# Kernel optimization log

Hardware: AMD Instinct MI355X
Metric: run time of the kernel (lower is better)

The kernel has to match this reference:

```python
import jax, jax.numpy as jnp
import numpy as np

B, N, C = 4, 2048, 768
H = 12
HD = C // H

def setup_inputs() -> dict:
    key = jax.random.key(0)
    k1, k2, k3, k4, k5 = jax.random.split(key, 5)
    x = jax.random.normal(k1, (B, N, C), dtype=jnp.float32)
    qkv_w = jax.random.normal(k2, (3 * C, C), dtype=jnp.float32) * (1.0 / np.sqrt(C))
    qkv_b = jax.random.normal(k3, (3 * C,), dtype=jnp.float32) * 0.02
    proj_w = jax.random.normal(k4, (C, C), dtype=jnp.float32) * (1.0 / np.sqrt(C))
    proj_b = jax.random.normal(k5, (C,), dtype=jnp.float32) * 0.02
    return {"x": x, "qkv_w": qkv_w, "qkv_b": qkv_b, "proj_w": proj_w, "proj_b": proj_b}

def reference(x, qkv_w, qkv_b, proj_w, proj_b):
    scale = HD ** (-0.5)
    # qkv projection: (B,N,3C)
    qkv = x @ qkv_w.T + qkv_b
    qkv = qkv.reshape(B, N, 3, H, HD).transpose(2, 0, 3, 1, 4)  # (3,B,H,N,HD)
    q, k, v = qkv[0], qkv[1], qkv[2]
    attn = jnp.einsum('bhqd,bhkd->bhqk', q, k) * scale  # (B,H,N,N)
    mask_value = -jnp.finfo(attn.dtype).max
    causal_mask = jnp.triu(jnp.ones((N, N), dtype=bool), k=1)
    attn = jnp.where(causal_mask, mask_value, attn)
    attn = jax.nn.softmax(attn, axis=-1)
    out = jnp.einsum('bhqk,bhkd->bhqd', attn, v)  # (B,H,N,HD)
    out = out.transpose(0, 2, 1, 3).reshape(B, N, C)
    return out @ proj_w.T + proj_b
```

## Files before the change

### kernel.cpp

```cpp
#include <hip/hip_runtime.h>
#include <hip/hip_bf16.h>


typedef __attribute__((ext_vector_type(8))) short bf16x8;
typedef __attribute__((ext_vector_type(4))) float f32x4;
typedef __attribute__((ext_vector_type(16))) float f32x16;

typedef __attribute__((address_space(3))) unsigned int lds_uint;
typedef __attribute__((address_space(1))) const unsigned int gbl_uint;

__device__ __forceinline__ void gload16(const void* g, void* l) {
  __builtin_amdgcn_global_load_lds((gbl_uint*)g, (lds_uint*)l, 16, 0, 0);
}

__device__ __forceinline__ unsigned short f2bf(float f) {
  unsigned u = __float_as_uint(f);
  unsigned rounding = 0x7FFFu + ((u >> 16) & 1u);
  return (unsigned short)((u + rounding) >> 16);
}

__device__ __forceinline__ unsigned cvtpk(float lo, float hi) {
  unsigned r;
  asm("v_cvt_pk_bf16_f32 %0, %1, %2" : "=v"(r) : "v"(lo), "v"(hi));
  return r;
}

__device__ __forceinline__ float exp2a(float x) {
  float r;
  asm("v_exp_f32 %0, %1" : "=v"(r) : "v"(x));
  return r;
}

__global__ void cast_weights(const float* __restrict__ qkv_w,
                             const float* __restrict__ proj_w,
                             unsigned short* __restrict__ qw,
                             unsigned short* __restrict__ pw) {
  const int idx = blockIdx.x * blockDim.x + threadIdx.x;
  const int stride = gridDim.x * blockDim.x;
  const int n1 = 2304 * 768, n2 = 768 * 768;
  for (int i = idx * 4; i < n1; i += stride * 4) {
    float4 v = *reinterpret_cast<const float4*>(qkv_w + i);
    ushort4 o;
    o.x = f2bf(v.x); o.y = f2bf(v.y); o.z = f2bf(v.z); o.w = f2bf(v.w);
    *reinterpret_cast<ushort4*>(qw + i) = o;
  }
  for (int i = idx * 4; i < n2; i += stride * 4) {
    float4 v = *reinterpret_cast<const float4*>(proj_w + i);
    ushort4 o;
    o.x = f2bf(v.x); o.y = f2bf(v.y); o.z = f2bf(v.z); o.w = f2bf(v.w);
    *reinterpret_cast<ushort4*>(pw + i) = o;
  }
}

template <bool OUT_F32, int BN, bool A_F32>
__global__ __launch_bounds__(256) void gemm_bt_kernel(
    const void* __restrict__ Avoid,
    const unsigned short* __restrict__ Bw,
    const float* __restrict__ bias,
    void* __restrict__ Cout,
    int M, int Ncols, int K, int ldc, int nblk) {
  constexpr int NFRAG = BN / 32;
  __shared__ __align__(16) short As[2][4096];
  __shared__ __align__(16) short Bs[2][BN * 32];

  const int t = threadIdx.x;
  const int lane = t & 63;
  const int wave = t >> 6;
  const int wm = wave >> 1;
  const int wn = wave & 1;

  const int wid = blockIdx.x;
  const int xcd = wid & 7;
  const int idx = wid >> 3;
  const int m0 = (xcd * 8 + idx / nblk) * 128;
  const int n0 = (idx % nblk) * BN;

  const int lrow = lane & 15;
  const int lk = (lane >> 4) * 8;

  const int srow = t >> 2, scol = (t & 3) * 8;
  const unsigned short* gA0 = nullptr;
  const unsigned short* gA1 = nullptr;
  const float* fA0 = nullptr;
  const float* fA1 = nullptr;
  if (A_F32) {
    fA0 = (const float*)Avoid + (size_t)(m0 + srow) * K + scol;
    fA1 = fA0 + (size_t)64 * K;
  } else {
    gA0 = (const unsigned short*)Avoid + (size_t)(m0 + srow) * K + scol;
    gA1 = gA0 + (size_t)64 * K;
  }
  const unsigned short* gB0 = Bw + (size_t)(n0 + srow) * K + scol;
  const unsigned short* gB1 = gB0 + (size_t)64 * K;
  const int db0 = wave * 512, db1 = 2048 + wave * 512;

  f32x4 acc[4][NFRAG] = {};
  const int nk = K / 32;

  if (A_F32) {
    float4 a0 = *reinterpret_cast<const float4*>(fA0);
    float4 a1 = *reinterpret_cast<const float4*>(fA0 + 4);
    float4 a2 = *reinterpret_cast<const float4*>(fA1);
    float4 a3 = *reinterpret_cast<const float4*>(fA1 + 4);
    uint4 w0, w1;
    w0.x = cvtpk(a0.x, a0.y); w0.y = cvtpk(a0.z, a0.w);
    w0.z = cvtpk(a1.x, a1.y); w0.w = cvtpk(a1.z, a1.w);
    w1.x = cvtpk(a2.x, a2.y); w1.y = cvtpk(a2.z, a2.w);
    w1.z = cvtpk(a3.x, a3.y); w1.w = cvtpk(a3.z, a3.w);
    *reinterpret_cast<uint4*>(&As[0][t * 8]) = w0;
    *reinterpret_cast<uint4*>(&As[0][2048 + t * 8]) = w1;
  } else {
    gload16(gA0, &As[0][db0]); gload16(gA1, &As[0][db1]);
  }
  gload16(gB0, &Bs[0][db0]);
  if (BN == 128) gload16(gB1, &Bs[0][db1]);

  int cur = 0;
  for (int kk = 0; kk < nk; ++kk) {
    __syncthreads();
    float4 a0 = {}, a1 = {}, a2 = {}, a3 = {};
    if (kk + 1 < nk) {
      const int off = (kk + 1) * 32;
      gload16(gB0 + off, &Bs[cur ^ 1][db0]);
      if (BN == 128) gload16(gB1 + off, &Bs[cur ^ 1][db1]);
      if (A_F32) {
        a0 = *reinterpret_cast<const float4*>(fA0 + off);
        a1 = *reinterpret_cast<const float4*>(fA0 + off + 4);
        a2 = *reinterpret_cast<const float4*>(fA1 + off);
        a3 = *reinterpret_cast<const float4*>(fA1 + off + 4);
      } else {
        gload16(gA0 + off, &As[cur ^ 1][db0]);
        gload16(gA1 + off, &As[cur ^ 1][db1]);
      }
    }
    bf16x8 a[4], b[NFRAG];
#pragma unroll
    for (int m = 0; m < 4; ++m)
      a[m] = *reinterpret_cast<const bf16x8*>(&As[cur][(wm * 64 + m * 16 + lrow) * 32 + lk]);
#pragma unroll
    for (int n = 0; n < NFRAG; ++n)
      b[n] = *reinterpret_cast<const bf16x8*>(&Bs[cur][(wn * (BN / 2) + n * 16 + lrow) * 32 + lk]);
#pragma unroll
    for (int m = 0; m < 4; ++m)
#pragma unroll
      for (int n = 0; n < NFRAG; ++n)
        acc[m][n] = __builtin_amdgcn_mfma_f32_16x16x32_bf16(a[m], b[n], acc[m][n], 0, 0, 0);
    if (A_F32 && kk + 1 < nk) {
      uint4 w0, w1;
      w0.x = cvtpk(a0.x, a0.y); w0.y = cvtpk(a0.z, a0.w);
      w0.z = cvtpk(a1.x, a1.y); w0.w = cvtpk(a1.z, a1.w);
      w1.x = cvtpk(a2.x, a2.y); w1.y = cvtpk(a2.z, a2.w);
      w1.z = cvtpk(a3.x, a3.y); w1.w = cvtpk(a3.z, a3.w);
      *reinterpret_cast<uint4*>(&As[cur ^ 1][t * 8]) = w0;
      *reinterpret_cast<uint4*>(&As[cur ^ 1][2048 + t * 8]) = w1;
    }
    cur ^= 1;
  }

  const int orow0 = (lane >> 4) * 4;
  const int ocol = lane & 15;
#pragma unroll
  for (int m = 0; m < 4; ++m) {
#pragma unroll
    for (int n = 0; n < NFRAG; ++n) {
      const int c = n0 + wn * (BN / 2) + n * 16 + ocol;
      const float bv = bias[c];
#pragma unroll
      for (int r = 0; r < 4; ++r) {
        const int rr = m0 + wm * 64 + m * 16 + orow0 + r;
        const float v = acc[m][n][r] + bv;
        if (OUT_F32)
          reinterpret_cast<float*>(Cout)[(size_t)rr * ldc + c] = v;
        else
          reinterpret_cast<unsigned short*>(Cout)[(size_t)rr * ldc + c] = f2bf(v);
      }
    }
  }
}

#define ATT_N 2048
#define ATT_H 12
#define QKV_LD 2304

__global__ __launch_bounds__(256) void transpose_v(
    const unsigned short* __restrict__ qkv, unsigned short* __restrict__ vt) {
  __shared__ __align__(16) short L[128 * 72];
  const int kb = blockIdx.x;
  const int bh = blockIdx.y;
  const int t = threadIdx.x;
  const int b = bh / ATT_H, h = bh % ATT_H;
  const int d0 = (t & 7) * 8;
  const int kl0 = t >> 3;
  const unsigned short* src =
      qkv + (size_t)(b * ATT_N + kb * 128) * QKV_LD + 1536 + h * 64 + d0;
#pragma unroll
  for (int r = 0; r < 4; ++r) {
    const int kl = kl0 + r * 32;
    bf16x8 v = *reinterpret_cast<const bf16x8*>(src + (size_t)kl * QKV_LD);
    *reinterpret_cast<bf16x8*>(&L[kl * 72 + d0]) = v;
  }
  __syncthreads();
  const int d = t >> 2;
  const int c = t & 3;
  unsigned short* dst = vt + (size_t)bh * 64 * ATT_N + (size_t)d * ATT_N + kb * 128;
#pragma unroll
  for (int cc = 0; cc < 4; ++cc) {
    const int kc = cc * 32 + c * 8;
    union { unsigned short s[8]; bf16x8 v; } U;
#pragma unroll
    for (int j = 0; j < 8; ++j) U.s[j] = (unsigned short)L[(kc + j) * 72 + d];
    *reinterpret_cast<bf16x8*>(dst + kc) = U.v;
  }
}

__global__ __launch_bounds__(256) void attn_kernel(
    const unsigned short* __restrict__ qkv,
    const unsigned short* __restrict__ vt,
    unsigned short* __restrict__ out) {
  __shared__ __align__(16) short Ks[2][4096];
  __shared__ __align__(16) short Vs[2][4096];

  const int t = threadIdx.x;
  const int lane = t & 63;
  const int w = t >> 6;
  const int hi = lane >> 5;
  const int l31 = lane & 31;

  const int wid = blockIdx.x;
  const int qb = 15 - (wid / 48);
  const int bh = wid % 48;
  const int b = bh / ATT_H;
  const int h = bh % ATT_H;

  const size_t rowbase = (size_t)b * ATT_N;
  const unsigned short* qptr = qkv + rowbase * QKV_LD + h * 64;
  const unsigned short* kptr = qptr + 768;
  const unsigned short* vtptr = vt + (size_t)bh * 64 * ATT_N;

  const int q0w = qb * 128 + w * 32;
  const int qg = q0w + l31;
  const int nt = (qb + 1) * 2;

  bf16x8 qf[4];
#pragma unroll
  for (int dk = 0; dk < 4; ++dk)
    qf[dk] = *reinterpret_cast<const bf16x8*>(
        qptr + (size_t)(q0w + l31) * QKV_LD + dk * 16 + hi * 8);

  f32x16 O0 = {}, O1 = {};
  float lrun = 0.f;

  int kKr[2], kKc[2];
#pragma unroll
  for (int c = 0; c < 2; ++c) {
    const int i = t + c * 256;
    const int f = i >> 6, ls = i & 63;
    kKr[c] = (f >> 2) * 32 + (ls & 31);
    kKc[c] = (f & 3) * 2 + (ls >> 5);
  }
  const unsigned short* gK0 = kptr + (size_t)kKr[0] * QKV_LD + kKc[0] * 8;
  const unsigned short* gK1 = kptr + (size_t)kKr[1] * QKV_LD + kKc[1] * 8;
  const unsigned short* gV0 = vtptr + (size_t)kKr[0] * ATT_N + kKc[0] * 8;
  const unsigned short* gV1 = vtptr + (size_t)kKr[1] * ATT_N + kKc[1] * 8;
  const int db0 = w * 512, db1 = 2048 + w * 512;

  gload16(gK0, &Ks[0][db0]); gload16(gK1, &Ks[0][db1]);
  gload16(gV0, &Vs[0][db0]); gload16(gV1, &Vs[0][db1]);

  int cur = 0;
  for (int kt = 0; kt < nt; ++kt) {
    const int k0 = kt * 64;
    __syncthreads();
    if (kt + 1 < nt) {
      const size_t advk = (size_t)(k0 + 64) * QKV_LD;
      gload16(gK0 + advk, &Ks[cur ^ 1][db0]); gload16(gK1 + advk, &Ks[cur ^ 1][db1]);
      gload16(gV0 + (k0 + 64), &Vs[cur ^ 1][db0]);
      gload16(gV1 + (k0 + 64), &Vs[cur ^ 1][db1]);
    }

    if (k0 <= q0w + 31) {
      f32x16 S0 = {}, S1 = {};
      __builtin_amdgcn_s_setprio(1);
#pragma unroll
      for (int dk = 0; dk < 4; ++dk) {
        bf16x8 kf = *reinterpret_cast<const bf16x8*>(&Ks[cur][(dk * 64 + lane) * 8]);
        S0 = __builtin_amdgcn_mfma_f32_32x32x16_bf16(kf, qf[dk], S0, 0, 0, 0);
      }
#pragma unroll
      for (int dk = 0; dk < 4; ++dk) {
        bf16x8 kf = *reinterpret_cast<const bf16x8*>(&Ks[cur][((4 + dk) * 64 + lane) * 8]);
        S1 = __builtin_amdgcn_mfma_f32_32x32x16_bf16(kf, qf[dk], S1, 0, 0, 0);
      }
      __builtin_amdgcn_s_setprio(0);

      const float scale2 = 0.18033688f;
      float p0[16], p1[16];
      if (k0 + 63 <= q0w) {
#pragma unroll
        for (int r = 0; r < 16; ++r) {
          p0[r] = exp2a(S0[r] * scale2);
          p1[r] = exp2a(S1[r] * scale2);
        }
      } else {
#pragma unroll
        for (int r = 0; r < 16; ++r) {
          int row = (r & 3) + 8 * (r >> 2) + 4 * hi;
          float e0 = (k0 + row > qg) ? -1e30f : S0[r] * scale2;
          float e1 = (k0 + 32 + row > qg) ? -1e30f : S1[r] * scale2;
          p0[r] = exp2a(e0);
          p1[r] = exp2a(e1);
        }
      }

      float sa = 0.f, sb = 0.f;
#pragma unroll
      for (int r = 0; r < 16; r += 2) { sa += p0[r] + p1[r]; sb += p0[r + 1] + p1[r + 1]; }
      float rsum = sa + sb;
      rsum += __shfl_xor(rsum, 32);
      lrun += rsum;

      bf16x8 Ub[4];
#pragma unroll
      for (int s = 0; s < 2; ++s) {
        unsigned pu[4][2];
#pragma unroll
        for (int m = 0; m < 4; ++m)
#pragma unroll
          for (int c = 0; c < 2; ++c)
            pu[m][c] = s ? cvtpk(p1[4 * m + 2 * c], p1[4 * m + 2 * c + 1])
                         : cvtpk(p0[4 * m + 2 * c], p0[4 * m + 2 * c + 1]);
#pragma unroll
        for (int tt = 0; tt < 2; ++tt) {
          unsigned s0v = hi ? pu[2 * tt][0] : pu[2 * tt + 1][0];
          unsigned s1v = hi ? pu[2 * tt][1] : pu[2 * tt + 1][1];
          unsigned r0 = __shfl_xor(s0v, 32);
          unsigned r1 = __shfl_xor(s1v, 32);
          union { unsigned u[4]; bf16x8 v; } U;
          U.u[0] = hi ? r0 : pu[2 * tt][0];
          U.u[1] = hi ? r1 : pu[2 * tt][1];
          U.u[2] = hi ? pu[2 * tt + 1][0] : r0;
          U.u[3] = hi ? pu[2 * tt + 1][1] : r1;
          Ub[s * 2 + tt] = U.v;
        }
      }

      __builtin_amdgcn_s_setprio(1);
#pragma unroll
      for (int ks = 0; ks < 4; ++ks) {
        bf16x8 vf0 = *reinterpret_cast<const bf16x8*>(&Vs[cur][(ks * 64 + lane) * 8]);
        O0 = __builtin_amdgcn_mfma_f32_32x32x16_bf16(vf0, Ub[ks], O0, 0, 0, 0);
        bf16x8 vf1 = *reinterpret_cast<const bf16x8*>(&Vs[cur][((4 + ks) * 64 + lane) * 8]);
        O1 = __builtin_amdgcn_mfma_f32_32x32x16_bf16(vf1, Ub[ks], O1, 0, 0, 0);
      }
      __builtin_amdgcn_s_setprio(0);
    }
    cur ^= 1;
  }

  const float inv = 1.0f / lrun;
  unsigned short* orow = out + (rowbase + q0w + l31) * 768 + h * 64;
#pragma unroll
  for (int half = 0; half < 2; ++half) {
    const f32x16& O = half ? O1 : O0;
#pragma unroll
    for (int m = 0; m < 4; ++m) {
      uint2 o2;
      o2.x = cvtpk(O[4 * m + 0] * inv, O[4 * m + 1] * inv);
      o2.y = cvtpk(O[4 * m + 2] * inv, O[4 * m + 3] * inv);
      *reinterpret_cast<uint2*>(orow + half * 32 + 8 * m + 4 * hi) = o2;
    }
  }
}

extern "C" void kernel_launch(void* const* d_in, const int* in_sizes, int n_in,
                              void* d_out, int out_size, void* d_ws, size_t ws_size,
                              hipStream_t stream) {
  const float* x = (const float*)d_in[0];
  const float* qkv_w = (const float*)d_in[1];
  const float* qkv_b = (const float*)d_in[2];
  const float* proj_w = (const float*)d_in[3];
  const float* proj_b = (const float*)d_in[4];
  float* out = (float*)d_out;

  unsigned short* qw_bf = (unsigned short*)d_ws;
  unsigned short* pw_bf = qw_bf + (size_t)2304 * 768;
  unsigned short* qkv = pw_bf + (size_t)768 * 768;
  unsigned short* attno = qkv + (size_t)8192 * 2304;
  unsigned short* vtb = attno + (size_t)8192 * 768;

  cast_weights<<<dim3(512), dim3(256), 0, stream>>>(qkv_w, proj_w, qw_bf, pw_bf);

  gemm_bt_kernel<false, 128, true><<<dim3(1152), dim3(256), 0, stream>>>(
      x, qw_bf, qkv_b, qkv, 8192, 2304, 768, 2304, 18);
  transpose_v<<<dim3(16, 48), dim3(256), 0, stream>>>(qkv, vtb);
  attn_kernel<<<dim3(768), dim3(256), 0, stream>>>(qkv, vtb, attno);
  gemm_bt_kernel<true, 64, false><<<dim3(768), dim3(256), 0, stream>>>(
      attno, pw_bf, proj_b, out, 8192, 768, 768, 768, 12);
}
```

Measured before the change: 147.5 us.

## Stage GEMM tiles through registers into padded single-buffer LDS

Replaces the double-buffered direct global-to-LDS loads with register prefetch of the next K-slice, followed by stores into a single LDS buffer padded to a row stride of 40 elements. The padding is meant to remove LDS bank conflicts on the fragment reads, and the smaller LDS footprint may allow higher occupancy. In exchange each K-step now needs two barriers instead of one, and data passes through VGPRs. The block-to-row mapping now derives rows per XCD from M instead of a hardcoded 8.

Result: faster. 142.5 us (median of 2 runs) (-3.4%).

```diff
diff --git a/kernel.cpp b/kernel.cpp
--- a/kernel.cpp
+++ b/kernel.cpp
@@ -60,8 +60,8 @@
     void* __restrict__ Cout,
     int M, int Ncols, int K, int ldc, int nblk) {
   constexpr int NFRAG = BN / 32;
-  __shared__ __align__(16) short As[2][4096];
-  __shared__ __align__(16) short Bs[2][BN * 32];
+  __shared__ __align__(16) short As[128 * 40];
+  __shared__ __align__(16) short Bs[BN * 40];
 
   const int t = threadIdx.x;
   const int lane = t & 63;
@@ -72,17 +72,16 @@
   const int wid = blockIdx.x;
   const int xcd = wid & 7;
   const int idx = wid >> 3;
-  const int m0 = (xcd * 8 + idx / nblk) * 128;
+  const int mpx = (M / 128) >> 3;
+  const int m0 = (xcd * mpx + idx / nblk) * 128;
   const int n0 = (idx % nblk) * BN;
 
   const int lrow = lane & 15;
   const int lk = (lane >> 4) * 8;
 
   const int srow = t >> 2, scol = (t & 3) * 8;
-  const unsigned short* gA0 = nullptr;
-  const unsigned short* gA1 = nullptr;
-  const float* fA0 = nullptr;
-  const float* fA1 = nullptr;
+  const float* fA0 = nullptr; const float* fA1 = nullptr;
+  const unsigned short* gA0 = nullptr; const unsigned short* gA1 = nullptr;
   if (A_F32) {
     fA0 = (const float*)Avoid + (size_t)(m0 + srow) * K + scol;
     fA1 = fA0 + (size_t)64 * K;
@@ -92,69 +91,71 @@
   }
   const unsigned short* gB0 = Bw + (size_t)(n0 + srow) * K + scol;
   const unsigned short* gB1 = gB0 + (size_t)64 * K;
-  const int db0 = wave * 512, db1 = 2048 + wave * 512;
 
   f32x4 acc[4][NFRAG] = {};
   const int nk = K / 32;
 
+  float4 ra0, ra1, ra2, ra3;
+  uint4 ua0, ua1;
+  uint4 ub0, ub1;
+
   if (A_F32) {
-    float4 a0 = *reinterpret_cast<const float4*>(fA0);
-    float4 a1 = *reinterpret_cast<const float4*>(fA0 + 4);
-    float4 a2 = *reinterpret_cast<const float4*>(fA1);
-    float4 a3 = *reinterpret_cast<const float4*>(fA1 + 4);
-    uint4 w0, w1;
-    w0.x = cvtpk(a0.x, a0.y); w0.y = cvtpk(a0.z, a0.w);
-    w0.z = cvtpk(a1.x, a1.y); w0.w = cvtpk(a1.z, a1.w);
-    w1.x = cvtpk(a2.x, a2.y); w1.y = cvtpk(a2.z, a2.w);
-    w1.z = cvtpk(a3.x, a3.y); w1.w = cvtpk(a3.z, a3.w);
-    *reinterpret_cast<uint4*>(&As[0][t * 8]) = w0;
-    *reinterpret_cast<uint4*>(&As[0][2048 + t * 8]) = w1;
+    ra0 = *reinterpret_cast<const float4*>(fA0);
+    ra1 = *reinterpret_cast<const float4*>(fA0 + 4);
+    ra2 = *reinterpret_cast<const float4*>(fA1);
+    ra3 = *reinterpret_cast<const float4*>(fA1 + 4);
   } else {
-    gload16(gA0, &As[0][db0]); gload16(gA1, &As[0][db1]);
-  }
-  gload16(gB0, &Bs[0][db0]);
-  if (BN == 128) gload16(gB1, &Bs[0][db1]);
-
-  int cur = 0;
+    ua0 = *reinterpret_cast<const uint4*>(gA0);
+    ua1 = *reinterpret_cast<const uint4*>(gA1);
+  }
+  ub0 = *reinterpret_cast<const uint4*>(gB0);
+  if (BN == 128) ub1 = *reinterpret_cast<const uint4*>(gB1);
+
   for (int kk = 0; kk < nk; ++kk) {
+    {
+      uint4 w0, w1;
+      if (A_F32) {
+        w0.x = cvtpk(ra0.x, ra0.y); w0.y = cvtpk(ra0.z, ra0.w);
+        w0.z = cvtpk(ra1.x, ra1.y); w0.w = cvtpk(ra1.z, ra1.w);
+        w1.x = cvtpk(ra2.x, ra2.y); w1.y = cvtpk(ra2.z, ra2.w);
+        w1.z = cvtpk(ra3.x, ra3.y); w1.w = cvtpk(ra3.z, ra3.w);
+      } else {
+        w0 = ua0; w1 = ua1;
+      }
+      *reinterpret_cast<uint4*>(&As[srow * 40 + scol]) = w0;
+      *reinterpret_cast<uint4*>(&As[(srow + 64) * 40 + scol]) = w1;
+      *reinterpret_cast<uint4*>(&Bs[srow * 40 + scol]) = ub0;
+      if (BN == 128)
+        *reinterpret_cast<uint4*>(&Bs[(srow + 64) * 40 + scol]) = ub1;
+    }
     __syncthreads();
-    float4 a0 = {}, a1 = {}, a2 = {}, a3 = {};
     if (kk + 1 < nk) {
       const int off = (kk + 1) * 32;
-      gload16(gB0 + off, &Bs[cur ^ 1][db0]);
-      if (BN == 128) gload16(gB1 + off, &Bs[cur ^ 1][db1]);
       if (A_F32) {
-        a0 = *reinterpret_cast<const float4*>(fA0 + off);
-        a1 = *reinterpret_cast<const float4*>(fA0 + off + 4);
-        a2 = *reinterpret_cast<const float4*>(fA1 + off);
-        a3 = *reinterpret_cast<const float4*>(fA1 + off + 4);
+        ra0 = *reinterpret_cast<const float4*>(fA0 + off);
+        ra1 = *reinterpret_cast<const float4*>(fA0 + off + 4);
+        ra2 = *reinterpret_cast<const float4*>(fA1 + off);
+        ra3 = *reinterpret_cast<const float4*>(fA1 + off + 4);
       } else {
-        gload16(gA0 + off, &As[cur ^ 1][db0]);
-        gload16(gA1 + off, &As[cur ^ 1][db1]);
-      }
+        ua0 = *reinterpret_cast<const uint4*>(gA0 + off);
+        ua1 = *reinterpret_cast<const uint4*>(gA1 + off);
+      }
+      ub0 = *reinterpret_cast<const uint4*>(gB0 + off);
+      if (BN == 128) ub1 = *reinterpret_cast<const uint4*>(gB1 + off);
     }
     bf16x8 a[4], b[NFRAG];
 #pragma unroll
     for (int m = 0; m < 4; ++m)
-      a[m] = *reinterpret_cast<const bf16x8*>(&As[cur][(wm * 64 + m * 16 + lrow) * 32 + lk]);
+      a[m] = *reinterpret_cast<const bf16x8*>(&As[(wm * 64 + m * 16 + lrow) * 40 + lk]);
 #pragma unroll
     for (int n = 0; n < NFRAG; ++n)
-      b[n] = *reinterpret_cast<const bf16x8*>(&Bs[cur][(wn * (BN / 2) + n * 16 + lrow) * 32 + lk]);
+      b[n] = *reinterpret_cast<const bf16x8*>(&Bs[(wn * (BN / 2) + n * 16 + lrow) * 40 + lk]);
 #pragma unroll
     for (int m = 0; m < 4; ++m)
 #pragma unroll
       for (int n = 0; n < NFRAG; ++n)
         acc[m][n] = __builtin_amdgcn_mfma_f32_16x16x32_bf16(a[m], b[n], acc[m][n], 0, 0, 0);
-    if (A_F32 && kk + 1 < nk) {
-      uint4 w0, w1;
-      w0.x = cvtpk(a0.x, a0.y); w0.y = cvtpk(a0.z, a0.w);
-      w0.z = cvtpk(a1.x, a1.y); w0.w = cvtpk(a1.z, a1.w);
-      w1.x = cvtpk(a2.x, a2.y); w1.y = cvtpk(a2.z, a2.w);
-      w1.z = cvtpk(a3.x, a3.y); w1.w = cvtpk(a3.z, a3.w);
-      *reinterpret_cast<uint4*>(&As[cur ^ 1][t * 8]) = w0;
-      *reinterpret_cast<uint4*>(&As[cur ^ 1][2048 + t * 8]) = w1;
-    }
-    cur ^= 1;
+    __syncthreads();
   }
 
   const int orow0 = (lane >> 4) * 4;
```
